# Kernel tuning notes

Measured on AMD Instinct MI355X. Metric: run time of the kernel, lower is better.

## Reference

```python
import jax, jax.numpy as jnp
import numpy as np

N_HEAD = 12

def setup_inputs() -> dict:
    key = jax.random.key(0)
    k1, k2, k3 = jax.random.split(key, 3)
    B, T, C = 8, 1024, 768
    x = jax.random.normal(k1, (B, T, C), dtype=jnp.float32)
    # Linear weights stored as [in, out] so y = x @ W + b (same math as torch Linear)
    w_attn = jax.random.normal(k2, (C, 3 * C), dtype=jnp.float32) * (1.0 / np.sqrt(C))
    b_attn = jnp.zeros((3 * C,), dtype=jnp.float32)
    w_proj = jax.random.normal(k3, (C, C), dtype=jnp.float32) * (1.0 / np.sqrt(C))
    b_proj = jnp.zeros((C,), dtype=jnp.float32)
    return {"x": x, "w_attn": w_attn, "b_attn": b_attn, "w_proj": w_proj, "b_proj": b_proj}

def reference(x, w_attn, b_attn, w_proj, b_proj):
    B, T, C = x.shape
    H = N_HEAD
    D = C // H
    qkv = x @ w_attn + b_attn                        # [B,T,3C]
    q, k, v = jnp.split(qkv, 3, axis=-1)             # each [B,T,C]
    q = q.reshape(B, T, H, D).transpose(0, 2, 1, 3)  # [B,H,T,D]
    k = k.reshape(B, T, H, D).transpose(0, 2, 1, 3)
    v = v.reshape(B, T, H, D).transpose(0, 2, 1, 3)
    scale = 1.0 / jnp.sqrt(jnp.asarray(D, dtype=x.dtype))
    att = jnp.einsum('bhqd,bhkd->bhqk', q, k) * scale  # [B,H,T,T]
    causal = jnp.tril(jnp.ones((T, T), dtype=bool))    # [T,T]
    att = jnp.where(causal[None, None], att, jnp.asarray(-jnp.inf, dtype=att.dtype))
    att = jax.nn.softmax(att, axis=-1)
    out = jnp.einsum('bhqk,bhkd->bhqd', att, v)        # [B,H,T,D]
    out = out.transpose(0, 2, 1, 3).reshape(B, T, C)
    return out @ w_proj + b_proj
```

## Files before the change

### kernel.cpp

```cpp
#include <hip/hip_runtime.h>
#include <hip/hip_bf16.h>
#include <cmath>

#define B_ 8
#define T_ 1024
#define C_ 768
#define H_ 12
#define D_ 64
#define N3C 2304
#define M_ 8192

typedef __bf16 bf16x4 __attribute__((ext_vector_type(4)));
typedef __bf16 bf16x8 __attribute__((ext_vector_type(8)));
typedef float  f32x4  __attribute__((ext_vector_type(4)));

typedef const __attribute__((address_space(1))) void* gptr_t;
typedef __attribute__((address_space(3))) void* lptr_t;

#define LOG2E 1.44269504088896f

__device__ __forceinline__ bf16x8 cvt_bf16x8(const float4& a, const float4& b) {
    bf16x8 r;
    r[0] = (__bf16)a.x; r[1] = (__bf16)a.y; r[2] = (__bf16)a.z; r[3] = (__bf16)a.w;
    r[4] = (__bf16)b.x; r[5] = (__bf16)b.y; r[6] = (__bf16)b.z; r[7] = (__bf16)b.w;
    return r;
}

__global__ __launch_bounds__(256) void prepass(const float* __restrict__ x,
                                               __bf16* __restrict__ xb,
                                               const float* __restrict__ wa,
                                               __bf16* __restrict__ wat,
                                               const float* __restrict__ wp,
                                               __bf16* __restrict__ wpt) {
    __shared__ float tile[32][33];
    const int bx = blockIdx.x, tid = threadIdx.x;
    if (bx < 3072) {
        int i = (bx * 256 + tid) * 8;
        float4 a = *(const float4*)&x[i];
        float4 b = *(const float4*)&x[i + 4];
        *(bf16x8*)&xb[i] = cvt_bf16x8(a, b);
        return;
    }
    const float* w;
    __bf16* wt;
    int K, N, n0, k0;
    if (bx < 4800) {
        int bb = bx - 3072;
        w = wa; wt = wat; K = 768; N = 2304;
        n0 = (bb % 72) * 32; k0 = (bb / 72) * 32;
    } else {
        int bb = bx - 4800;
        w = wp; wt = wpt; K = 768; N = 768;
        n0 = (bb % 24) * 32; k0 = (bb / 24) * 32;
    }
    int tx = tid & 31, ty = tid >> 5;
#pragma unroll
    for (int i = 0; i < 4; i++)
        tile[ty + i * 8][tx] = w[(size_t)(k0 + ty + i * 8) * N + n0 + tx];
    __syncthreads();
#pragma unroll
    for (int i = 0; i < 4; i++)
        wt[(size_t)(n0 + ty + i * 8) * K + k0 + tx] = (__bf16)tile[tx][ty + i * 8];
}

__global__ __launch_bounds__(512, 2) void qkv_gemm_mfma(const __bf16* __restrict__ A,
                                                        const __bf16* __restrict__ Bt,
                                                        const float* __restrict__ bias,
                                                        __bf16* __restrict__ qb,
                                                        __bf16* __restrict__ kb,
                                                        __bf16* __restrict__ vbt) {
    __shared__ __bf16 smem[73728];
    __bf16* Abuf = smem;
    __bf16* Bbuf = smem + 49152;
    const int tid = threadIdx.x;
    const int wave = tid >> 6, lane = tid & 63;
    const int lane15 = lane & 15, quad = lane >> 4;
    const int swz = (blockIdx.x & 7) * 72 + (blockIdx.x >> 3);
    const int n0 = (swz % 18) * 128;
    const int m0 = (swz / 18) * 256;
    const int wm = (wave >> 1) * 64, wn = (wave & 1) * 64;
    f32x4 acc[4][4] = {};

#define ISSUE_A2(KC, R0)                                                            \
    {                                                                               \
        const int k0s = (KC) * 64;                                                  \
        __bf16* Ad = Abuf + ((KC) % 3) * 16384;                                     \
        _Pragma("unroll")                                                           \
        for (int r = (R0); r < (R0) + 2; ++r) {                                     \
            int p = r * 512 + tid;                                                  \
            int row = p >> 3, csw = p & 7;                                          \
            __builtin_amdgcn_global_load_lds(                                       \
                (gptr_t)(A + (size_t)(m0 + row) * 768 + k0s + (csw ^ (row & 7)) * 8), \
                (lptr_t)(Ad + (r * 512 + wave * 64) * 8), 16, 0, 0);                \
        }                                                                           \
    }

#define ISSUE_B1(KC, R0)                                                            \
    {                                                                               \
        const int k0s = (KC) * 64;                                                  \
        __bf16* Bd = Bbuf + ((KC) % 3) * 8192;                                      \
        int p = (R0) * 512 + tid;                                                   \
        int row = p >> 3, csw = p & 7;                                              \
        __builtin_amdgcn_global_load_lds(                                           \
            (gptr_t)(Bt + (size_t)(n0 + row) * 768 + k0s + (csw ^ (row & 7)) * 8),  \
            (lptr_t)(Bd + ((R0) * 512 + wave * 64) * 8), 16, 0, 0);                 \
    }

#define BAR() asm volatile("s_barrier" ::: "memory")

    ISSUE_A2(0, 0); ISSUE_A2(0, 2); ISSUE_B1(0, 0); ISSUE_B1(0, 1);
    ISSUE_A2(1, 0); ISSUE_A2(1, 2); ISSUE_B1(1, 0); ISSUE_B1(1, 1);

    for (int kc = 0; kc < 12; ++kc) {
        if (kc < 11) { asm volatile("s_waitcnt vmcnt(6)" ::: "memory"); }
        else         { asm volatile("s_waitcnt vmcnt(0)" ::: "memory"); }
        BAR();
        const __bf16* Ac = Abuf + (kc % 3) * 16384;
        const __bf16* Bc = Bbuf + (kc % 3) * 8192;
        const bool pf = (kc + 2 < 12);

        bf16x8 af[4], bfr[2];
#pragma unroll
        for (int mt = 0; mt < 4; ++mt) {
            int m = wm + mt * 16 + lane15;
            af[mt] = *(const bf16x8*)(Ac + m * 64 + (quad ^ (m & 7)) * 8);
        }
#pragma unroll
        for (int nt = 0; nt < 2; ++nt) {
            int n = wn + nt * 16 + lane15;
            bfr[nt] = *(const bf16x8*)(Bc + n * 64 + (quad ^ (n & 7)) * 8);
        }
        if (pf) ISSUE_A2(kc + 2, 0);
        BAR();
        __builtin_amdgcn_s_setprio(1);
#pragma unroll
        for (int mt = 0; mt < 4; ++mt)
#pragma unroll
            for (int nt = 0; nt < 2; ++nt)
                acc[mt][nt] = __builtin_amdgcn_mfma_f32_16x16x32_bf16(af[mt], bfr[nt], acc[mt][nt], 0, 0, 0);
        __builtin_amdgcn_s_setprio(0);

#pragma unroll
        for (int nt = 0; nt < 2; ++nt) {
            int n = wn + (2 + nt) * 16 + lane15;
            bfr[nt] = *(const bf16x8*)(Bc + n * 64 + (quad ^ (n & 7)) * 8);
        }
        if (pf) ISSUE_A2(kc + 2, 2);
        BAR();
        __builtin_amdgcn_s_setprio(1);
#pragma unroll
        for (int mt = 0; mt < 4; ++mt)
#pragma unroll
            for (int nt = 0; nt < 2; ++nt)
                acc[mt][2 + nt] = __builtin_amdgcn_mfma_f32_16x16x32_bf16(af[mt], bfr[nt], acc[mt][2 + nt], 0, 0, 0);
        __builtin_amdgcn_s_setprio(0);

#pragma unroll
        for (int mt = 0; mt < 4; ++mt) {
            int m = wm + mt * 16 + lane15;
            af[mt] = *(const bf16x8*)(Ac + m * 64 + ((4 + quad) ^ (m & 7)) * 8);
        }
#pragma unroll
        for (int nt = 0; nt < 2; ++nt) {
            int n = wn + nt * 16 + lane15;
            bfr[nt] = *(const bf16x8*)(Bc + n * 64 + ((4 + quad) ^ (n & 7)) * 8);
        }
        if (pf) ISSUE_B1(kc + 2, 0);
        BAR();
        __builtin_amdgcn_s_setprio(1);
#pragma unroll
        for (int mt = 0; mt < 4; ++mt)
#pragma unroll
            for (int nt = 0; nt < 2; ++nt)
                acc[mt][nt] = __builtin_amdgcn_mfma_f32_16x16x32_bf16(af[mt], bfr[nt], acc[mt][nt], 0, 0, 0);
        __builtin_amdgcn_s_setprio(0);

#pragma unroll
        for (int nt = 0; nt < 2; ++nt) {
            int n = wn + (2 + nt) * 16 + lane15;
            bfr[nt] = *(const bf16x8*)(Bc + n * 64 + ((4 + quad) ^ (n & 7)) * 8);
        }
        if (pf) ISSUE_B1(kc + 2, 1);
        BAR();
        __builtin_amdgcn_s_setprio(1);
#pragma unroll
        for (int mt = 0; mt < 4; ++mt)
#pragma unroll
            for (int nt = 0; nt < 2; ++nt)
                acc[mt][2 + nt] = __builtin_amdgcn_mfma_f32_16x16x32_bf16(af[mt], bfr[nt], acc[mt][2 + nt], 0, 0, 0);
        __builtin_amdgcn_s_setprio(0);
    }

    if (n0 < 1536) {
        const bool isq = (n0 < 768);
        const float sc = isq ? (0.125f * LOG2E) : 1.0f;
#pragma unroll
        for (int nt = 0; nt < 4; ++nt) {
            int n = n0 + wn + nt * 16 + lane15;
            int rem = isq ? n : (n - 768);
            int h = rem >> 6;
            int d = n & 63;
            float bv = bias[n];
            __bf16* dst = isq ? qb : kb;
#pragma unroll
            for (int mt = 0; mt < 4; ++mt) {
#pragma unroll
                for (int reg = 0; reg < 4; ++reg) {
                    int mr = m0 + wm + mt * 16 + quad * 4 + reg;
                    int bb = mr >> 10, t = mr & 1023;
                    dst[(((size_t)bb * H_ + h) * T_ + t) * D_ + d] =
                        (__bf16)((acc[mt][nt][reg] + bv) * sc);
                }
            }
        }
    } else {
        __bf16* vls = smem;
#pragma unroll
        for (int nt = 0; nt < 4; ++nt) {
            int nl = wn + nt * 16 + lane15;
            float bv = bias[n0 + nl];
#pragma unroll
            for (int mt = 0; mt < 4; ++mt)
#pragma unroll
                for (int reg = 0; reg < 4; ++reg)
                    vls[nl * 264 + wm + mt * 16 + quad * 4 + reg] =
                        (__bf16)(acc[mt][nt][reg] + bv);
        }
        __syncthreads();
        int nl = tid >> 2;
        int t0 = (tid & 3) * 64;
        int n = n0 + nl;
        int h = (n - 1536) >> 6;
        int d = n & 63;
        int bb = m0 >> 10, tg = (m0 & 1023) + t0;
        __bf16* dst = vbt + (((size_t)bb * H_ + h) * D_ + d) * T_ + tg;
        const __bf16* srcl = vls + nl * 264 + t0;
#pragma unroll
        for (int c = 0; c < 8; ++c) {
            bf16x8 v;
#pragma unroll
            for (int i = 0; i < 8; ++i) {
                int s = c * 8 + i;
                v[i] = srcl[(s & 3) * 16 + (s >> 2)];
            }
            *(bf16x8*)(dst + c * 8) = v;
        }
    }
#undef ISSUE_A2
#undef ISSUE_B1
#undef BAR
}

__global__ __launch_bounds__(256) void proj_gemm_mfma(const __bf16* __restrict__ A,
                                                      const __bf16* __restrict__ Bt,
                                                      const float* __restrict__ bias,
                                                      float* __restrict__ out) {
    __shared__ __bf16 As[128 * 64];
    __shared__ __bf16 Bs[64 * 64];
    const int tid = threadIdx.x;
    const int wave = tid >> 6, lane = tid & 63;
    const int lane15 = lane & 15, quad = lane >> 4;
    const int bid = blockIdx.x;
    const int m0 = ((bid & 7) * 8 + ((bid >> 3) & 7)) * 128;
    const int n0 = (bid >> 6) * 64;
    const int wm = wave * 32;
    f32x4 acc[2][4] = {};

#define PSTAGE(KC)                                                                  \
    {                                                                               \
        const int k0s = (KC) * 64;                                                  \
        _Pragma("unroll")                                                           \
        for (int r = 0; r < 4; ++r) {                                               \
            int p = r * 256 + tid;                                                  \
            int mrow = p >> 3, csw = p & 7;                                         \
            int ksrc = (csw ^ (mrow & 7)) * 8;                                      \
            __builtin_amdgcn_global_load_lds(                                       \
                (gptr_t)(A + (size_t)(m0 + mrow) * 768 + k0s + ksrc),               \
                (lptr_t)(&As[0] + (r * 256 + wave * 64) * 8), 16, 0, 0);            \
        }                                                                           \
        _Pragma("unroll")                                                           \
        for (int r = 0; r < 2; ++r) {                                               \
            int p = r * 256 + tid;                                                  \
            int nrow = p >> 3, csw = p & 7;                                         \
            int ksrc = (csw ^ (nrow & 7)) * 8;                                      \
            __builtin_amdgcn_global_load_lds(                                       \
                (gptr_t)(Bt + (size_t)(n0 + nrow) * 768 + k0s + ksrc),              \
                (lptr_t)(&Bs[0] + (r * 256 + wave * 64) * 8), 16, 0, 0);            \
        }                                                                           \
    }

    for (int kc = 0; kc < 12; ++kc) {
        PSTAGE(kc);
        __syncthreads();
#pragma unroll
        for (int ks = 0; ks < 2; ++ks) {
            bf16x8 af[2], bf[4];
#pragma unroll
            for (int mt = 0; mt < 2; ++mt) {
                int m = wm + mt * 16 + lane15;
                int csw = (ks * 4 + quad) ^ (m & 7);
                af[mt] = *(const bf16x8*)(&As[0] + m * 64 + csw * 8);
            }
#pragma unroll
            for (int nt = 0; nt < 4; ++nt) {
                int n = nt * 16 + lane15;
                int csw = (ks * 4 + quad) ^ (n & 7);
                bf[nt] = *(const bf16x8*)(&Bs[0] + n * 64 + csw * 8);
            }
#pragma unroll
            for (int mt = 0; mt < 2; ++mt)
#pragma unroll
                for (int nt = 0; nt < 4; ++nt)
                    acc[mt][nt] = __builtin_amdgcn_mfma_f32_16x16x32_bf16(af[mt], bf[nt], acc[mt][nt], 0, 0, 0);
        }
        __syncthreads();
    }

#pragma unroll
    for (int nt = 0; nt < 4; ++nt) {
        int n = n0 + nt * 16 + lane15;
        float bv = bias[n];
#pragma unroll
        for (int mt = 0; mt < 2; ++mt) {
#pragma unroll
            for (int reg = 0; reg < 4; ++reg) {
                int mr = m0 + wm + mt * 16 + quad * 4 + reg;
                out[(size_t)mr * C_ + n] = acc[mt][nt][reg] + bv;
            }
        }
    }
}

__global__ __launch_bounds__(256) void attn_mfma(const __bf16* __restrict__ qb,
                                                 const __bf16* __restrict__ kb,
                                                 const __bf16* __restrict__ vbt,
                                                 __bf16* __restrict__ ao) {
    __shared__ __bf16 Ks[2][64 * 64];
    __shared__ __bf16 Vts[2][64 * 64];
    __shared__ __bf16 Ps[4 * 32 * 72];

    const int tid = threadIdx.x;
    const int wave = tid >> 6, lane = tid & 63;
    const int lane15 = lane & 15, quad = lane >> 4;
    const int bh = blockIdx.x;
    const int qt = 7 - blockIdx.y;
    const int b = bh / H_, h = bh % H_;
    const int q0 = qt * 128;

    const __bf16* Kb = kb + (size_t)bh * T_ * D_;
    const __bf16* Vb = vbt + (size_t)bh * D_ * T_;
    __bf16* Pw = Ps + wave * 32 * 72;

    bf16x8 qf[2][2];
#pragma unroll
    for (int g = 0; g < 2; ++g) {
        const __bf16* qrow = qb + ((size_t)bh * T_ + q0 + wave * 32 + g * 16 + lane15) * D_ + quad * 8;
        qf[g][0] = *(const bf16x8*)qrow;
        qf[g][1] = *(const bf16x8*)(qrow + 32);
    }

    f32x4 o[2][4] = {};
    float lsum[2][4] = {};

    const int kunits = 2 * qt + 2;

#define ASTAGE(KU, BUF)                                                            \
    {                                                                              \
        const int k0s = (KU) * 64;                                                 \
        _Pragma("unroll")                                                          \
        for (int r = 0; r < 2; ++r) {                                              \
            int p = r * 256 + tid;                                                 \
            int row = p >> 3, c = p & 7;                                           \
            int cs = (c ^ (row & 7)) * 8;                                          \
            __builtin_amdgcn_global_load_lds(                                      \
                (gptr_t)(Kb + (size_t)(k0s + row) * D_ + cs),                      \
                (lptr_t)(&Ks[BUF][0] + (r * 256 + wave * 64) * 8), 16, 0, 0);      \
            __builtin_amdgcn_global_load_lds(                                      \
                (gptr_t)(Vb + (size_t)row * T_ + k0s + cs),                        \
                (lptr_t)(&Vts[BUF][0] + (r * 256 + wave * 64) * 8), 16, 0, 0);     \
        }                                                                          \
    }

    ASTAGE(0, 0);

    for (int ku = 0; ku < kunits; ++ku) {
        __syncthreads();
        if (ku + 1 < kunits) ASTAGE(ku + 1, (ku + 1) & 1);
        const __bf16* Kc = &Ks[ku & 1][0];
        const __bf16* Vc = &Vts[ku & 1][0];
        const int k0 = ku * 64;

        f32x4 s[2][4];
#pragma unroll
        for (int kt = 0; kt < 4; ++kt) {
            int row = kt * 16 + lane15;
            bf16x8 kf0 = *(const bf16x8*)(Kc + row * 64 + ((quad) ^ (row & 7)) * 8);
            bf16x8 kf1 = *(const bf16x8*)(Kc + row * 64 + ((4 + quad) ^ (row & 7)) * 8);
#pragma unroll
            for (int g = 0; g < 2; ++g) {
                f32x4 t = {};
                t = __builtin_amdgcn_mfma_f32_16x16x32_bf16(qf[g][0], kf0, t, 0, 0, 0);
                t = __builtin_amdgcn_mfma_f32_16x16x32_bf16(qf[g][1], kf1, t, 0, 0, 0);
                s[g][kt] = t;
            }
        }

        const bool diag = (ku >= 2 * qt);
#pragma unroll
        for (int g = 0; g < 2; ++g) {
#pragma unroll
            for (int r = 0; r < 4; ++r) {
                bf16x4 pk;
#pragma unroll
                for (int kt = 0; kt < 4; ++kt) {
                    int col = k0 + kt * 16 + lane15;
                    float p = __builtin_amdgcn_exp2f(s[g][kt][r]);
                    if (diag) {
                        int qrow = q0 + wave * 32 + g * 16 + quad * 4 + r;
                        if (col > qrow) p = 0.f;
                    }
                    lsum[g][r] += p;
                    pk[kt] = (__bf16)p;
                }
                *(bf16x4*)(Pw + (g * 16 + quad * 4 + r) * 72 + lane15 * 4) = pk;
            }
        }

        bf16x8 vf[4][2];
#pragma unroll
        for (int dt = 0; dt < 4; ++dt) {
            int row = dt * 16 + lane15;
#pragma unroll
            for (int half = 0; half < 2; ++half)
                vf[dt][half] = *(const bf16x8*)(Vc + row * 64 + ((half * 4 + quad) ^ (row & 7)) * 8);
        }
#pragma unroll
        for (int g = 0; g < 2; ++g) {
#pragma unroll
            for (int half = 0; half < 2; ++half) {
                bf16x8 pf = *(const bf16x8*)(Pw + (g * 16 + lane15) * 72 + half * 32 + quad * 8);
#pragma unroll
                for (int dt = 0; dt < 4; ++dt)
                    o[g][dt] = __builtin_amdgcn_mfma_f32_16x16x32_bf16(pf, vf[dt][half], o[g][dt], 0, 0, 0);
            }
        }
    }

#pragma unroll
    for (int g = 0; g < 2; ++g) {
        float inv[4];
#pragma unroll
        for (int r = 0; r < 4; ++r) {
            float ls = lsum[g][r];
            ls += __shfl_xor(ls, 1);
            ls += __shfl_xor(ls, 2);
            ls += __shfl_xor(ls, 4);
            ls += __shfl_xor(ls, 8);
            inv[r] = 1.0f / ls;
        }
#pragma unroll
        for (int dt = 0; dt < 4; ++dt) {
#pragma unroll
            for (int r = 0; r < 4; ++r) {
                int t = q0 + wave * 32 + g * 16 + quad * 4 + r;
                ao[((size_t)(b * T_ + t)) * C_ + h * 64 + dt * 16 + lane15] =
                    (__bf16)(o[g][dt][r] * inv[r]);
            }
        }
    }
}

extern "C" void kernel_launch(void* const* d_in, const int* in_sizes, int n_in,
                              void* d_out, int out_size, void* d_ws, size_t ws_size,
                              hipStream_t stream) {
    const float* x = (const float*)d_in[0];
    const float* w_attn = (const float*)d_in[1];
    const float* b_attn = (const float*)d_in[2];
    const float* w_proj = (const float*)d_in[3];
    const float* b_proj = (const float*)d_in[4];
    float* out = (float*)d_out;

    __bf16* xb = (__bf16*)d_ws;
    __bf16* wat = xb + (size_t)M_ * C_;
    __bf16* wpt = wat + (size_t)N3C * C_;
    __bf16* qb = wpt + (size_t)C_ * C_;
    __bf16* kb = qb + (size_t)96 * T_ * D_;
    __bf16* vbt = kb + (size_t)96 * T_ * D_;
    __bf16* ao = vbt + (size_t)96 * T_ * D_;

    prepass<<<5376, 256, 0, stream>>>(x, xb, w_attn, wat, w_proj, wpt);
    qkv_gemm_mfma<<<576, 512, 0, stream>>>(xb, wat, b_attn, qb, kb, vbt);
    attn_mfma<<<dim3(96, 8), 256, 0, stream>>>(qb, kb, vbt, ao);
    proj_gemm_mfma<<<768, 256, 0, stream>>>(ao, wpt, b_proj, out);
}
```

Measured before the change: 170.4 us.

## Triple-buffer projection GEMM with split-phase prefetch and MFMA priority hints

```diff
diff --git a/kernel.cpp b/kernel.cpp
--- a/kernel.cpp
+++ b/kernel.cpp
@@ -214,6 +214,7 @@
             }
         }
     } else {
+        __syncthreads();
         __bf16* vls = smem;
 #pragma unroll
         for (int nt = 0; nt < 4; ++nt) {
@@ -255,8 +256,8 @@
                                                       const __bf16* __restrict__ Bt,
                                                       const float* __restrict__ bias,
                                                       float* __restrict__ out) {
-    __shared__ __bf16 As[128 * 64];
-    __shared__ __bf16 Bs[64 * 64];
+    __shared__ __bf16 As[3][128 * 64];
+    __shared__ __bf16 Bs[3][64 * 64];
     const int tid = threadIdx.x;
     const int wave = tid >> 6, lane = tid & 63;
     const int lane15 = lane & 15, quad = lane >> 4;
@@ -266,54 +267,91 @@
     const int wm = wave * 32;
     f32x4 acc[2][4] = {};
 
-#define PSTAGE(KC)                                                                  \
+#define PISSUE_A(KC)                                                                \
     {                                                                               \
         const int k0s = (KC) * 64;                                                  \
+        __bf16* Ad = &As[(KC) % 3][0];                                              \
         _Pragma("unroll")                                                           \
         for (int r = 0; r < 4; ++r) {                                               \
             int p = r * 256 + tid;                                                  \
-            int mrow = p >> 3, csw = p & 7;                                         \
-            int ksrc = (csw ^ (mrow & 7)) * 8;                                      \
+            int row = p >> 3, csw = p & 7;                                          \
             __builtin_amdgcn_global_load_lds(                                       \
-                (gptr_t)(A + (size_t)(m0 + mrow) * 768 + k0s + ksrc),               \
-                (lptr_t)(&As[0] + (r * 256 + wave * 64) * 8), 16, 0, 0);            \
+                (gptr_t)(A + (size_t)(m0 + row) * 768 + k0s + (csw ^ (row & 7)) * 8), \
+                (lptr_t)(Ad + (r * 256 + wave * 64) * 8), 16, 0, 0);                \
         }                                                                           \
+    }
+
+#define PISSUE_B(KC)                                                                \
+    {                                                                               \
+        const int k0s = (KC) * 64;                                                  \
+        __bf16* Bd = &Bs[(KC) % 3][0];                                              \
         _Pragma("unroll")                                                           \
         for (int r = 0; r < 2; ++r) {                                               \
             int p = r * 256 + tid;                                                  \
-            int nrow = p >> 3, csw = p & 7;                                         \
-            int ksrc = (csw ^ (nrow & 7)) * 8;                                      \
+            int row = p >> 3, csw = p & 7;                                          \
             __builtin_amdgcn_global_load_lds(                                       \
-                (gptr_t)(Bt + (size_t)(n0 + nrow) * 768 + k0s + ksrc),              \
-                (lptr_t)(&Bs[0] + (r * 256 + wave * 64) * 8), 16, 0, 0);            \
+                (gptr_t)(Bt + (size_t)(n0 + row) * 768 + k0s + (csw ^ (row & 7)) * 8), \
+                (lptr_t)(Bd + (r * 256 + wave * 64) * 8), 16, 0, 0);                \
         }                                                                           \
     }
 
+#define PBAR() asm volatile("s_barrier" ::: "memory")
+
+    PISSUE_A(0); PISSUE_B(0);
+    PISSUE_A(1); PISSUE_B(1);
+
     for (int kc = 0; kc < 12; ++kc) {
-        PSTAGE(kc);
-        __syncthreads();
-#pragma unroll
-        for (int ks = 0; ks < 2; ++ks) {
+        if (kc < 11) { asm volatile("s_waitcnt vmcnt(6)" ::: "memory"); }
+        else         { asm volatile("s_waitcnt vmcnt(0)" ::: "memory"); }
+        PBAR();
+        const __bf16* Ac = &As[kc % 3][0];
+        const __bf16* Bc = &Bs[kc % 3][0];
+        const bool pf = (kc + 2 < 12);
+
+        {
             bf16x8 af[2], bf[4];
 #pragma unroll
             for (int mt = 0; mt < 2; ++mt) {
                 int m = wm + mt * 16 + lane15;
-                int csw = (ks * 4 + quad) ^ (m & 7);
-                af[mt] = *(const bf16x8*)(&As[0] + m * 64 + csw * 8);
+                af[mt] = *(const bf16x8*)(Ac + m * 64 + (quad ^ (m & 7)) * 8);
             }
 #pragma unroll
             for (int nt = 0; nt < 4; ++nt) {
                 int n = nt * 16 + lane15;
-                int csw = (ks * 4 + quad) ^ (n & 7);
-                bf[nt] = *(const bf16x8*)(&Bs[0] + n * 64 + csw * 8);
-            }
+                bf[nt] = *(const bf16x8*)(Bc + n * 64 + (quad ^ (n & 7)) * 8);
+            }
+            if (pf) PISSUE_A(kc + 2);
+            PBAR();
+            __builtin_amdgcn_s_setprio(1);
 #pragma unroll
             for (int mt = 0; mt < 2; ++mt)
 #pragma unroll
                 for (int nt = 0; nt < 4; ++nt)
                     acc[mt][nt] = __builtin_amdgcn_mfma_f32_16x16x32_bf16(af[mt], bf[nt], acc[mt][nt], 0, 0, 0);
-        }
-        __syncthreads();
+            __builtin_amdgcn_s_setprio(0);
+        }
+        {
+            bf16x8 af[2], bf[4];
+#pragma unroll
+            for (int mt = 0; mt < 2; ++mt) {
+                int m = wm + mt * 16 + lane15;
+                af[mt] = *(const bf16x8*)(Ac + m * 64 + ((4 + quad) ^ (m & 7)) * 8);
+            }
+#pragma unroll
+            for (int nt = 0; nt < 4; ++nt) {
+                int n = nt * 16 + lane15;
+                bf[nt] = *(const bf16x8*)(Bc + n * 64 + ((4 + quad) ^ (n & 7)) * 8);
+            }
+            if (pf) PISSUE_B(kc + 2);
+            PBAR();
+            __builtin_amdgcn_s_setprio(1);
+#pragma unroll
+            for (int mt = 0; mt < 2; ++mt)
+#pragma unroll
+                for (int nt = 0; nt < 4; ++nt)
+                    acc[mt][nt] = __builtin_amdgcn_mfma_f32_16x16x32_bf16(af[mt], bf[nt], acc[mt][nt], 0, 0, 0);
+            __builtin_amdgcn_s_setprio(0);
+        }
     }
 
 #pragma unroll
@@ -329,6 +367,9 @@
             }
         }
     }
+#undef PISSUE_A
+#undef PISSUE_B
+#undef PBAR
 }
 
 __global__ __launch_bounds__(256) void attn_mfma(const __bf16* __restrict__ qb,
@@ -391,6 +432,7 @@
         const int k0 = ku * 64;
 
         f32x4 s[2][4];
+        __builtin_amdgcn_s_setprio(1);
 #pragma unroll
         for (int kt = 0; kt < 4; ++kt) {
             int row = kt * 16 + lane15;
@@ -404,6 +446,7 @@
                 s[g][kt] = t;
             }
         }
+        __builtin_amdgcn_s_setprio(0);
 
         const bool diag = (ku >= 2 * qt);
 #pragma unroll
@@ -434,6 +477,7 @@
             for (int half = 0; half < 2; ++half)
                 vf[dt][half] = *(const bf16x8*)(Vc + row * 64 + ((half * 4 + quad) ^ (row & 7)) * 8);
         }
+        __builtin_amdgcn_s_setprio(1);
 #pragma unroll
         for (int g = 0; g < 2; ++g) {
 #pragma unroll
@@ -444,6 +488,7 @@
                     o[g][dt] = __builtin_amdgcn_mfma_f32_16x16x32_bf16(pf, vf[dt][half], o[g][dt], 0, 0, 0);
             }
         }
+        __builtin_amdgcn_s_setprio(0);
     }
 
 #pragma unroll
```

New measurement: 177.1 us. +3.9%, slower.

## Pair light and heavy causal query tiles per attention block for balance

Applied to the files above, without the earlier changes.

```diff
diff --git a/kernel.cpp b/kernel.cpp
--- a/kernel.cpp
+++ b/kernel.cpp
@@ -214,6 +214,7 @@
             }
         }
     } else {
+        __syncthreads();
         __bf16* vls = smem;
 #pragma unroll
         for (int nt = 0; nt < 4; ++nt) {
@@ -329,6 +330,7 @@
             }
         }
     }
+#undef PSTAGE
 }
 
 __global__ __launch_bounds__(256) void attn_mfma(const __bf16* __restrict__ qb,
@@ -337,36 +339,39 @@
                                                  __bf16* __restrict__ ao) {
     __shared__ __bf16 Ks[2][64 * 64];
     __shared__ __bf16 Vts[2][64 * 64];
-    __shared__ __bf16 Ps[4 * 32 * 72];
+    __shared__ __bf16 Ps[4 * 16 * 72];
 
     const int tid = threadIdx.x;
     const int wave = tid >> 6, lane = tid & 63;
     const int lane15 = lane & 15, quad = lane >> 4;
     const int bh = blockIdx.x;
-    const int qt = 7 - blockIdx.y;
+    const int y = blockIdx.y;
+    const int qtA = 15 - y;
+    const int qtB = y;
+    const int kuA = qtA + 1;
+    const int UT = 17;
     const int b = bh / H_, h = bh % H_;
-    const int q0 = qt * 128;
 
     const __bf16* Kb = kb + (size_t)bh * T_ * D_;
     const __bf16* Vb = vbt + (size_t)bh * D_ * T_;
-    __bf16* Pw = Ps + wave * 32 * 72;
-
-    bf16x8 qf[2][2];
-#pragma unroll
-    for (int g = 0; g < 2; ++g) {
-        const __bf16* qrow = qb + ((size_t)bh * T_ + q0 + wave * 32 + g * 16 + lane15) * D_ + quad * 8;
-        qf[g][0] = *(const bf16x8*)qrow;
-        qf[g][1] = *(const bf16x8*)(qrow + 32);
-    }
-
-    f32x4 o[2][4] = {};
-    float lsum[2][4] = {};
-
-    const int kunits = 2 * qt + 2;
-
-#define ASTAGE(KU, BUF)                                                            \
+    __bf16* Pw = Ps + wave * 16 * 72;
+
+    bf16x8 qfA[2], qfB[2];
+    {
+        const __bf16* qrA = qb + ((size_t)bh * T_ + qtA * 64 + wave * 16 + lane15) * D_ + quad * 8;
+        qfA[0] = *(const bf16x8*)qrA;
+        qfA[1] = *(const bf16x8*)(qrA + 32);
+        const __bf16* qrB = qb + ((size_t)bh * T_ + qtB * 64 + wave * 16 + lane15) * D_ + quad * 8;
+        qfB[0] = *(const bf16x8*)qrB;
+        qfB[1] = *(const bf16x8*)(qrB + 32);
+    }
+
+    f32x4 o[4] = {};
+    float lsum[4] = {0.f, 0.f, 0.f, 0.f};
+
+#define ASTAGE(K0S, BUF)                                                           \
     {                                                                              \
-        const int k0s = (KU) * 64;                                                 \
+        const int k0s = (K0S);                                                     \
         _Pragma("unroll")                                                          \
         for (int r = 0; r < 2; ++r) {                                              \
             int p = r * 256 + tid;                                                 \
@@ -383,47 +388,52 @@
 
     ASTAGE(0, 0);
 
-    for (int ku = 0; ku < kunits; ++ku) {
+    for (int u = 0; u < UT; ++u) {
+        const int seg = (u >= kuA) ? 1 : 0;
+        const int qt = seg ? qtB : qtA;
+        const int k0 = (seg ? (u - kuA) : u) * 64;
         __syncthreads();
-        if (ku + 1 < kunits) ASTAGE(ku + 1, (ku + 1) & 1);
-        const __bf16* Kc = &Ks[ku & 1][0];
-        const __bf16* Vc = &Vts[ku & 1][0];
-        const int k0 = ku * 64;
-
-        f32x4 s[2][4];
+        if (u + 1 < UT) {
+            const int un = u + 1;
+            const int k0n = (un < kuA) ? un * 64 : (un - kuA) * 64;
+            ASTAGE(k0n, un & 1);
+        }
+        const __bf16* Kc = &Ks[u & 1][0];
+        const __bf16* Vc = &Vts[u & 1][0];
+
+        const bf16x8 q0r = seg ? qfB[0] : qfA[0];
+        const bf16x8 q1r = seg ? qfB[1] : qfA[1];
+
+        f32x4 s[4];
+        __builtin_amdgcn_s_setprio(1);
 #pragma unroll
         for (int kt = 0; kt < 4; ++kt) {
             int row = kt * 16 + lane15;
             bf16x8 kf0 = *(const bf16x8*)(Kc + row * 64 + ((quad) ^ (row & 7)) * 8);
             bf16x8 kf1 = *(const bf16x8*)(Kc + row * 64 + ((4 + quad) ^ (row & 7)) * 8);
-#pragma unroll
-            for (int g = 0; g < 2; ++g) {
-                f32x4 t = {};
-                t = __builtin_amdgcn_mfma_f32_16x16x32_bf16(qf[g][0], kf0, t, 0, 0, 0);
-                t = __builtin_amdgcn_mfma_f32_16x16x32_bf16(qf[g][1], kf1, t, 0, 0, 0);
-                s[g][kt] = t;
-            }
-        }
-
-        const bool diag = (ku >= 2 * qt);
-#pragma unroll
-        for (int g = 0; g < 2; ++g) {
-#pragma unroll
-            for (int r = 0; r < 4; ++r) {
-                bf16x4 pk;
-#pragma unroll
-                for (int kt = 0; kt < 4; ++kt) {
-                    int col = k0 + kt * 16 + lane15;
-                    float p = __builtin_amdgcn_exp2f(s[g][kt][r]);
-                    if (diag) {
-                        int qrow = q0 + wave * 32 + g * 16 + quad * 4 + r;
-                        if (col > qrow) p = 0.f;
-                    }
-                    lsum[g][r] += p;
-                    pk[kt] = (__bf16)p;
+            f32x4 t = {};
+            t = __builtin_amdgcn_mfma_f32_16x16x32_bf16(q0r, kf0, t, 0, 0, 0);
+            t = __builtin_amdgcn_mfma_f32_16x16x32_bf16(q1r, kf1, t, 0, 0, 0);
+            s[kt] = t;
+        }
+        __builtin_amdgcn_s_setprio(0);
+
+        const bool diag = (k0 == qt * 64);
+#pragma unroll
+        for (int r = 0; r < 4; ++r) {
+            bf16x4 pk;
+#pragma unroll
+            for (int kt = 0; kt < 4; ++kt) {
+                int col = k0 + kt * 16 + lane15;
+                float p = __builtin_amdgcn_exp2f(s[kt][r]);
+                if (diag) {
+                    int qrow = qt * 64 + wave * 16 + quad * 4 + r;
+                    if (col > qrow) p = 0.f;
                 }
-                *(bf16x4*)(Pw + (g * 16 + quad * 4 + r) * 72 + lane15 * 4) = pk;
-            }
+                lsum[r] += p;
+                pk[kt] = (__bf16)p;
+            }
+            *(bf16x4*)(Pw + (quad * 4 + r) * 72 + lane15 * 4) = pk;
         }
 
         bf16x8 vf[4][2];
@@ -434,40 +444,42 @@
             for (int half = 0; half < 2; ++half)
                 vf[dt][half] = *(const bf16x8*)(Vc + row * 64 + ((half * 4 + quad) ^ (row & 7)) * 8);
         }
-#pragma unroll
-        for (int g = 0; g < 2; ++g) {
-#pragma unroll
-            for (int half = 0; half < 2; ++half) {
-                bf16x8 pf = *(const bf16x8*)(Pw + (g * 16 + lane15) * 72 + half * 32 + quad * 8);
-#pragma unroll
-                for (int dt = 0; dt < 4; ++dt)
-                    o[g][dt] = __builtin_amdgcn_mfma_f32_16x16x32_bf16(pf, vf[dt][half], o[g][dt], 0, 0, 0);
-            }
-        }
-    }
-
-#pragma unroll
-    for (int g = 0; g < 2; ++g) {
-        float inv[4];
-#pragma unroll
-        for (int r = 0; r < 4; ++r) {
-            float ls = lsum[g][r];
-            ls += __shfl_xor(ls, 1);
-            ls += __shfl_xor(ls, 2);
-            ls += __shfl_xor(ls, 4);
-            ls += __shfl_xor(ls, 8);
-            inv[r] = 1.0f / ls;
-        }
-#pragma unroll
-        for (int dt = 0; dt < 4; ++dt) {
+        __builtin_amdgcn_s_setprio(1);
+#pragma unroll
+        for (int half = 0; half < 2; ++half) {
+            bf16x8 pf = *(const bf16x8*)(Pw + lane15 * 72 + half * 32 + quad * 8);
+#pragma unroll
+            for (int dt = 0; dt < 4; ++dt)
+                o[dt] = __builtin_amdgcn_mfma_f32_16x16x32_bf16(pf, vf[dt][half], o[dt], 0, 0, 0);
+        }
+        __builtin_amdgcn_s_setprio(0);
+
+        if (u == kuA - 1 || u == UT - 1) {
+            const int q0 = qt * 64;
+            float inv[4];
 #pragma unroll
             for (int r = 0; r < 4; ++r) {
-                int t = q0 + wave * 32 + g * 16 + quad * 4 + r;
-                ao[((size_t)(b * T_ + t)) * C_ + h * 64 + dt * 16 + lane15] =
-                    (__bf16)(o[g][dt][r] * inv[r]);
-            }
-        }
-    }
+                float ls = lsum[r];
+                ls += __shfl_xor(ls, 1);
+                ls += __shfl_xor(ls, 2);
+                ls += __shfl_xor(ls, 4);
+                ls += __shfl_xor(ls, 8);
+                inv[r] = 1.0f / ls;
+                lsum[r] = 0.f;
+            }
+#pragma unroll
+            for (int dt = 0; dt < 4; ++dt) {
+#pragma unroll
+                for (int r = 0; r < 4; ++r) {
+                    int t = q0 + wave * 16 + quad * 4 + r;
+                    ao[((size_t)(b * T_ + t)) * C_ + h * 64 + dt * 16 + lane15] =
+                        (__bf16)(o[dt][r] * inv[r]);
+                }
+                o[dt] = f32x4{};
+            }
+        }
+    }
+#undef ASTAGE
 }
 
 extern "C" void kernel_launch(void* const* d_in, const int* in_sizes, int n_in,
```

New measurement: 168.9 us, median of 4. Within noise of the previous version (-0.8%).
